# Kernel tuning notes

Hardware: AMD Instinct MI355X
Metric: run time of the kernel (lower is better)

Reference implementation:

```python
import jax, jax.numpy as jnp
import numpy as np

B, T, F, H = 128, 512, 256, 512


def setup_inputs() -> dict:
    key = jax.random.key(0)
    k1, k2, k3, k4 = jax.random.split(key, 4)
    scale_k = 1.0 / np.sqrt(F)
    scale_r = 1.0 / np.sqrt(H)
    return {
        "x": jax.random.normal(k1, (B, T, F), dtype=jnp.float32),
        "kernel": jax.random.normal(k2, (F, 4 * H), dtype=jnp.float32) * scale_k,
        "recurrent_kernel": jax.random.normal(k3, (H, 4 * H), dtype=jnp.float32) * scale_r,
        "bias": jax.random.normal(k4, (4 * H,), dtype=jnp.float32) * 0.01,
    }


def _lstm(x, kernel, recurrent_kernel, bias):
    # x: [B, T, F] -> scan over time. Keras gate order: i, f, g(cell), o.
    h0 = jnp.zeros((x.shape[0], H), dtype=x.dtype)
    c0 = jnp.zeros((x.shape[0], H), dtype=x.dtype)
    # Precompute input projections for all timesteps in one big GEMM: [B,T,4H]
    xz = jnp.einsum('btf,fg->btg', x, kernel) + bias

    def step(carry, xz_t):
        h, c = carry
        z = xz_t + h @ recurrent_kernel  # [B, 4H]
        i, f, g, o = jnp.split(z, 4, axis=-1)
        i = jax.nn.sigmoid(i)
        f = jax.nn.sigmoid(f)
        g = jnp.tanh(g)
        o = jax.nn.sigmoid(o)
        c_new = f * c + i * g
        h_new = o * jnp.tanh(c_new)
        return (h_new, c_new), h_new

    (h_last, c_last), hs = jax.lax.scan(step, (h0, c0), jnp.swapaxes(xz, 0, 1))
    output = jnp.swapaxes(hs, 0, 1)  # [B, T, H]
    return output, h_last, c_last


def reference(x, kernel, recurrent_kernel, bias):
    # Inference-mode forward (dropout inactive), matching Keras LSTM eval behavior.
    output, h, c = _lstm(x, kernel, recurrent_kernel, bias)
    return (output, h, c)
```

## Files before the change

kernel.cpp:

```cpp
#include <hip/hip_runtime.h>
#include <stdint.h>


#define Bb 128
#define Tt 512
#define Ff 256
#define Hh 512
#define G4 2048
#define SENT 0xFFFFFFFFu

typedef __attribute__((ext_vector_type(8))) short short8;
typedef __attribute__((ext_vector_type(4))) float floatx4;
typedef __attribute__((ext_vector_type(4))) unsigned int uint4v;

__device__ __forceinline__ unsigned short f2bf(float f) {
    unsigned u = __float_as_uint(f);
    return (unsigned short)((u + 0x7FFFu + ((u >> 16) & 1u)) >> 16);
}
__device__ __forceinline__ float bf2f(unsigned short h) {
    return __uint_as_float(((unsigned)h) << 16);
}
__device__ __forceinline__ float sigm(float x) { return 1.f / (1.f + __expf(-x)); }
__device__ __forceinline__ float tanh_f(float x) {
    float e = __expf(-2.f * fabsf(x));
    return copysignf((1.f - e) / (1.f + e), x);
}

__global__ __launch_bounds__(256, 2) void lstm_xz(
    const float* __restrict__ x, const float* __restrict__ w,
    const float* __restrict__ bias, _Float16* __restrict__ xzh)
{
    __shared__ unsigned short Ahi[128 * 40];
    __shared__ unsigned short Alo[128 * 40];
    __shared__ unsigned short Wt [128 * 40];

    const int tid = threadIdx.x;
    int idx = blockIdx.x;
    int xcd = idx & 7;
    int chunk = idx >> 3;
    int msup = chunk >> 7;
    int s = chunk & 127;
    int nt = s >> 3;
    int mi0 = s & 7;
    int mt = xcd * 64 + msup * 8 + mi0;
    const int m0 = mt << 7;
    const int n0 = nt << 7;

    const int lane = tid & 63;
    const int wv = tid >> 6;
    const int wm = wv >> 1, wn = wv & 1;
    const int cB = lane & 15, kgrp = lane >> 4;

    floatx4 acc[4][4];
#pragma unroll
    for (int i = 0; i < 4; ++i)
#pragma unroll
        for (int j = 0; j < 4; ++j) acc[i][j] = (floatx4){0.f, 0.f, 0.f, 0.f};

    float bv[4];
#pragma unroll
    for (int ni = 0; ni < 4; ++ni) bv[ni] = bias[n0 + wn * 64 + ni * 16 + cB];

    for (int it = 0; it < 8; ++it) {
        const int k0 = it * 32;
#pragma unroll
        for (int sw = 0; sw < 4; ++sw) {
            int e = sw * 256 + tid;
            int row = e >> 3, kq = e & 7;
            float4 v = *((const float4*)(x + (size_t)(m0 + row) * Ff + k0) + kq);
            unsigned short h0 = f2bf(v.x), h1 = f2bf(v.y), h2 = f2bf(v.z), h3 = f2bf(v.w);
            unsigned short l0 = f2bf(v.x - bf2f(h0)), l1 = f2bf(v.y - bf2f(h1));
            unsigned short l2 = f2bf(v.z - bf2f(h2)), l3 = f2bf(v.w - bf2f(h3));
            uint2 ph, pl;
            ph.x = (unsigned)h0 | ((unsigned)h1 << 16); ph.y = (unsigned)h2 | ((unsigned)h3 << 16);
            pl.x = (unsigned)l0 | ((unsigned)l1 << 16); pl.y = (unsigned)l2 | ((unsigned)l3 << 16);
            *(uint2*)(&Ahi[row * 40 + kq * 4]) = ph;
            *(uint2*)(&Alo[row * 40 + kq * 4]) = pl;
        }
#pragma unroll
        for (int sw = 0; sw < 4; ++sw) {
            int e = sw * 256 + tid;
            int kr = e >> 5, nq = e & 31;
            float4 v = *((const float4*)(w + (size_t)(k0 + kr) * G4 + n0) + nq);
            int nb = nq * 4;
            Wt[(nb + 0) * 40 + kr] = f2bf(v.x);
            Wt[(nb + 1) * 40 + kr] = f2bf(v.y);
            Wt[(nb + 2) * 40 + kr] = f2bf(v.z);
            Wt[(nb + 3) * 40 + kr] = f2bf(v.w);
        }
        __syncthreads();

        short8 bfr[4];
#pragma unroll
        for (int ni = 0; ni < 4; ++ni)
            bfr[ni] = *(const short8*)(&Wt[(wn * 64 + ni * 16 + cB) * 40 + kgrp * 8]);
#pragma unroll
        for (int mi = 0; mi < 4; ++mi) {
            short8 ah = *(const short8*)(&Ahi[(wm * 64 + mi * 16 + cB) * 40 + kgrp * 8]);
            short8 al = *(const short8*)(&Alo[(wm * 64 + mi * 16 + cB) * 40 + kgrp * 8]);
#pragma unroll
            for (int ni = 0; ni < 4; ++ni) {
                acc[mi][ni] = __builtin_amdgcn_mfma_f32_16x16x32_bf16(ah, bfr[ni], acc[mi][ni], 0, 0, 0);
                acc[mi][ni] = __builtin_amdgcn_mfma_f32_16x16x32_bf16(al, bfr[ni], acc[mi][ni], 0, 0, 0);
            }
        }
        __syncthreads();
    }
#pragma unroll
    for (int mi = 0; mi < 4; ++mi)
#pragma unroll
        for (int ni = 0; ni < 4; ++ni) {
            int rowb = m0 + wm * 64 + mi * 16 + kgrp * 4;
            int col = n0 + wn * 64 + ni * 16 + cB;
#pragma unroll
            for (int rr = 0; rr < 4; ++rr)
                xzh[(size_t)(rowb + rr) * G4 + col] = (_Float16)(acc[mi][ni][rr] + bv[ni]);
        }
}

__global__ __launch_bounds__(256, 1) void lstm_rec(
    const _Float16* __restrict__ xzh, const float* __restrict__ rk,
    unsigned* __restrict__ hbuf_u, float* __restrict__ out)
{
    __shared__ unsigned short Rlds[128 * 512];
    __shared__ unsigned short hlds[16 * 512];

    const int tid = threadIdx.x;
    const int idx = blockIdx.x;
    const int rg = idx & 7;
    const int cb = idx >> 3;
    const int b0 = rg * 16;
    const int hc0 = cb * 32;

    const int lane = tid & 63;
    const int wv = tid >> 6;
    const int cB = lane & 15, kgrp = lane >> 4;
    const int hcw = hc0 + wv * 8;
    const int c7 = cB & 7;
    const int col = hcw + c7;
    const bool hi = (cB & 8) != 0;

    for (int e = tid; e < 64 * 512; e += 256) {
        int p = e & 63, k = e >> 6;
        int n0 = 2 * p;
        int loc = n0 & 31, w = n0 >> 5;
        int gate = ((loc >> 4) << 1) | ((loc >> 3) & 1);
        int gcol = gate * Hh + hc0 + w * 8 + (loc & 7);
        float2 v = *(const float2*)(rk + (size_t)k * G4 + gcol);
        Rlds[n0 * 512 + (k ^ ((n0 & 7) << 3))] = f2bf(v.x);
        Rlds[(n0 + 1) * 512 + (k ^ (((n0 + 1) & 7) << 3))] = f2bf(v.y);
    }

    const unsigned* xz_u = (const unsigned*)xzh;
    const unsigned* pr[4];
#pragma unroll
    for (int r = 0; r < 4; ++r)
        pr[r] = xz_u + ((size_t)(b0 + kgrp * 4 + r) * Tt * G4 + (col & ~1)) / 2;

    float xzr[16];
#pragma unroll
    for (int g = 0; g < 4; ++g)
#pragma unroll
        for (int r = 0; r < 4; ++r) {
            unsigned v = pr[r][g * 256];
            xzr[g * 4 + r] = (float)__builtin_bit_cast(_Float16,
                (unsigned short)((col & 1) ? (v >> 16) : (v & 0xffffu)));
        }
#pragma unroll
    for (int r = 0; r < 4; ++r) pr[r] += G4 / 2;

    __syncthreads();

    short8 bf0[16], bf1[16];
    {
        const int nb = wv * 32;
        const int swz = c7 << 3;
#pragma unroll
        for (int kk = 0; kk < 16; ++kk) {
            int kb = (kk * 32 + kgrp * 8) ^ swz;
            bf0[kk] = *(const short8*)&Rlds[(nb + cB) * 512 + kb];
            bf1[kk] = *(const short8*)&Rlds[(nb + 16 + cB) * 512 + kb];
        }
    }

    float creg[4] = {0.f, 0.f, 0.f, 0.f};
    unsigned* hlds_u = (unsigned*)hlds;
    unsigned* const gbase = hbuf_u + (size_t)rg * 4 * 4096;

    for (int t = 0; t < Tt; ++t) {
        const bool last = (t == Tt - 1);

        unsigned pf[16];
        if (!last) {
#pragma unroll
            for (int g = 0; g < 4; ++g)
#pragma unroll
                for (int r = 0; r < 4; ++r)
                    pf[g * 4 + r] = pr[r][g * 256];
        }

        floatx4 acc0 = (floatx4){0.f, 0.f, 0.f, 0.f};
        floatx4 acc1 = (floatx4){0.f, 0.f, 0.f, 0.f};

        if (t > 0) {
            const unsigned* sb = gbase + ((t - 1) & 3) * 4096;
            const unsigned* p0 = sb + (wv + 0) * 256 + 4 * lane;
            const unsigned* p1 = sb + (wv + 4) * 256 + 4 * lane;
            const unsigned* p2 = sb + (wv + 8) * 256 + 4 * lane;
            const unsigned* p3 = sb + (wv + 12) * 256 + 4 * lane;
            uint4v v0, v1, v2, v3;
            for (;;) {
                asm volatile("global_load_dwordx4 %0, %1, off sc0 sc1" : "=v"(v0) : "v"(p0) : "memory");
                asm volatile("global_load_dwordx4 %0, %1, off sc0 sc1" : "=v"(v1) : "v"(p1) : "memory");
                asm volatile("global_load_dwordx4 %0, %1, off sc0 sc1" : "=v"(v2) : "v"(p2) : "memory");
                asm volatile("global_load_dwordx4 %0, %1, off sc0 sc1" : "=v"(v3) : "v"(p3) : "memory");
                asm volatile("s_waitcnt vmcnt(0)" ::: "memory");
                bool bad = (v0[0] == SENT) | (v0[1] == SENT) | (v0[2] == SENT) | (v0[3] == SENT)
                         | (v1[0] == SENT) | (v1[1] == SENT) | (v1[2] == SENT) | (v1[3] == SENT)
                         | (v2[0] == SENT) | (v2[1] == SENT) | (v2[2] == SENT) | (v2[3] == SENT)
                         | (v3[0] == SENT) | (v3[1] == SENT) | (v3[2] == SENT) | (v3[3] == SENT);
                if (!bad) break;
            }
            __builtin_amdgcn_sched_barrier(0);
            *(uint4v*)(hlds_u + (wv + 0) * 256 + 4 * (lane ^ ((wv + 0) & 7))) = v0;
            *(uint4v*)(hlds_u + (wv + 4) * 256 + 4 * (lane ^ ((wv + 4) & 7))) = v1;
            *(uint4v*)(hlds_u + (wv + 8) * 256 + 4 * (lane ^ ((wv + 8) & 7))) = v2;
            *(uint4v*)(hlds_u + (wv + 12) * 256 + 4 * (lane ^ ((wv + 12) & 7))) = v3;
            __syncthreads();

            if (t >= 2) {
                unsigned* rs = gbase + ((t - 2) & 3) * 4096
                             + (tid >> 4) * 256 + (hc0 >> 1) + (tid & 15);
                __hip_atomic_store(rs, SENT, __ATOMIC_RELAXED, __HIP_MEMORY_SCOPE_AGENT);
            }

            const int swz = c7 << 3;
#pragma unroll
            for (int kk = 0; kk < 16; ++kk) {
                int kb = (kk * 32 + kgrp * 8) ^ swz;
                short8 a = *(const short8*)&hlds[cB * 512 + kb];
                acc0 = __builtin_amdgcn_mfma_f32_16x16x32_bf16(a, bf0[kk], acc0, 0, 0, 0);
                acc1 = __builtin_amdgcn_mfma_f32_16x16x32_bf16(a, bf1[kk], acc1, 0, 0, 0);
            }
        }

        float hv[4];
#pragma unroll
        for (int r = 0; r < 4; ++r) {
            float a0 = acc0[r], a1 = acc1[r];
            float a0x = __shfl_xor(a0, 8);
            float a1x = __shfl_xor(a1, 8);
            float zi = (hi ? a0x : a0) + xzr[0 * 4 + r];
            float zf = (hi ? a0 : a0x) + xzr[1 * 4 + r];
            float zg = (hi ? a1x : a1) + xzr[2 * 4 + r];
            float zo = (hi ? a1 : a1x) + xzr[3 * 4 + r];
            creg[r] = sigm(zf) * creg[r] + sigm(zi) * tanh_f(zg);
            hv[r] = sigm(zo) * tanh_f(creg[r]);
        }

        float hn[4];
#pragma unroll
        for (int r = 0; r < 4; ++r) hn[r] = __shfl_xor(hv[r], 1);
        const bool ew = (!hi && !(cB & 1));

        if (!last) {
            unsigned* wbase = gbase + (t & 3) * 4096;
#pragma unroll
            for (int r = 0; r < 4; ++r) {
                if (ew) {
                    unsigned hp = (unsigned)f2bf(hv[r]) | ((unsigned)f2bf(hn[r]) << 16);
                    __hip_atomic_store(wbase + (kgrp * 4 + r) * 256 + (col >> 1), hp,
                                       __ATOMIC_RELAXED, __HIP_MEMORY_SCOPE_AGENT);
                }
            }
        }

#pragma unroll
        for (int r = 0; r < 4; ++r) {
            if (ew) {
                size_t b = (size_t)(b0 + kgrp * 4 + r);
                *(float2*)(out + (b * Tt + (size_t)t) * Hh + col) = make_float2(hv[r], hn[r]);
            }
        }

        if (last) {
            float* hl = out + (size_t)Bb * Tt * Hh;
            float* cl = hl + (size_t)Bb * Hh;
#pragma unroll
            for (int r = 0; r < 4; ++r) {
                float cn = __shfl_xor(creg[r], 1);
                if (ew) {
                    size_t b = (size_t)(b0 + kgrp * 4 + r);
                    *(float2*)(hl + b * Hh + col) = make_float2(hv[r], hn[r]);
                    *(float2*)(cl + b * Hh + col) = make_float2(creg[r], cn);
                }
            }
            break;
        }

#pragma unroll
        for (int i = 0; i < 16; ++i)
            xzr[i] = (float)__builtin_bit_cast(_Float16,
                (unsigned short)((col & 1) ? (pf[i] >> 16) : (pf[i] & 0xffffu)));
#pragma unroll
        for (int r = 0; r < 4; ++r) pr[r] += G4 / 2;

        __syncthreads();
    }
}

extern "C" void kernel_launch(void* const* d_in, const int* in_sizes, int n_in,
                              void* d_out, int out_size, void* d_ws, size_t ws_size,
                              hipStream_t stream) {
    (void)in_sizes; (void)n_in; (void)out_size; (void)ws_size;
    const float* x    = (const float*)d_in[0];
    const float* w    = (const float*)d_in[1];
    const float* rk   = (const float*)d_in[2];
    const float* bias = (const float*)d_in[3];
    float* out = (float*)d_out;

    char* ws = (char*)d_ws;
    const size_t XZ_BYTES   = (size_t)Bb * Tt * G4 * sizeof(_Float16);
    const size_t HBUF_BYTES = (size_t)8 * 4 * 16 * 256 * 4;

    _Float16* xzh = (_Float16*)ws;
    unsigned* hbuf = (unsigned*)(ws + XZ_BYTES);

    hipMemsetAsync(ws + XZ_BYTES, 0xFF, HBUF_BYTES, stream);

    lstm_xz<<<dim3(8192), dim3(256), 0, stream>>>(x, w, bias, xzh);
    lstm_rec<<<dim3(128), dim3(256), 0, stream>>>(xzh, rk, hbuf, out);
}
```

Measured before the change: 2.203 ms.

## Load h operands directly from global into MFMA registers, drop LDS staging and barriers

Each wave now loads its full 16x512 bf16 h fragment straight from the global exchange buffer into registers in MFMA A-operand layout. This replaces the cooperative load, LDS store and __syncthreads. The per-step block barriers are removed, and sentinel polling becomes a wave-wide __any check. The goal is to cut the LDS round trip and the two block-wide synchronizations on the serial recurrent critical path. In exchange each wave issues four times more global loads (redundantly across the 4 waves) and holds 64 more VGPRs. The sentinel reset indexing was changed to match the new ownership.

```diff
diff --git a/kernel.cpp b/kernel.cpp
--- a/kernel.cpp
+++ b/kernel.cpp
@@ -123,7 +123,6 @@
     unsigned* __restrict__ hbuf_u, float* __restrict__ out)
 {
     __shared__ unsigned short Rlds[128 * 512];
-    __shared__ unsigned short hlds[16 * 512];
 
     const int tid = threadIdx.x;
     const int idx = blockIdx.x;
@@ -184,7 +183,6 @@
     }
 
     float creg[4] = {0.f, 0.f, 0.f, 0.f};
-    unsigned* hlds_u = (unsigned*)hlds;
     unsigned* const gbase = hbuf_u + (size_t)rg * 4 * 4096;
 
     for (int t = 0; t < Tt; ++t) {
@@ -203,42 +201,32 @@
         floatx4 acc1 = (floatx4){0.f, 0.f, 0.f, 0.f};
 
         if (t > 0) {
-            const unsigned* sb = gbase + ((t - 1) & 3) * 4096;
-            const unsigned* p0 = sb + (wv + 0) * 256 + 4 * lane;
-            const unsigned* p1 = sb + (wv + 4) * 256 + 4 * lane;
-            const unsigned* p2 = sb + (wv + 8) * 256 + 4 * lane;
-            const unsigned* p3 = sb + (wv + 12) * 256 + 4 * lane;
-            uint4v v0, v1, v2, v3;
+            const unsigned* sp = gbase + ((t - 1) & 3) * 4096 + cB * 256 + kgrp * 4;
+            uint4v A[16];
             for (;;) {
-                asm volatile("global_load_dwordx4 %0, %1, off sc0 sc1" : "=v"(v0) : "v"(p0) : "memory");
-                asm volatile("global_load_dwordx4 %0, %1, off sc0 sc1" : "=v"(v1) : "v"(p1) : "memory");
-                asm volatile("global_load_dwordx4 %0, %1, off sc0 sc1" : "=v"(v2) : "v"(p2) : "memory");
-                asm volatile("global_load_dwordx4 %0, %1, off sc0 sc1" : "=v"(v3) : "v"(p3) : "memory");
+#pragma unroll
+                for (int kk = 0; kk < 16; ++kk)
+                    asm volatile("global_load_dwordx4 %0, %1, off sc0 sc1"
+                                 : "=v"(A[kk]) : "v"(sp + kk * 16) : "memory");
                 asm volatile("s_waitcnt vmcnt(0)" ::: "memory");
-                bool bad = (v0[0] == SENT) | (v0[1] == SENT) | (v0[2] == SENT) | (v0[3] == SENT)
-                         | (v1[0] == SENT) | (v1[1] == SENT) | (v1[2] == SENT) | (v1[3] == SENT)
-                         | (v2[0] == SENT) | (v2[1] == SENT) | (v2[2] == SENT) | (v2[3] == SENT)
-                         | (v3[0] == SENT) | (v3[1] == SENT) | (v3[2] == SENT) | (v3[3] == SENT);
-                if (!bad) break;
-            }
-            __builtin_amdgcn_sched_barrier(0);
-            *(uint4v*)(hlds_u + (wv + 0) * 256 + 4 * (lane ^ ((wv + 0) & 7))) = v0;
-            *(uint4v*)(hlds_u + (wv + 4) * 256 + 4 * (lane ^ ((wv + 4) & 7))) = v1;
-            *(uint4v*)(hlds_u + (wv + 8) * 256 + 4 * (lane ^ ((wv + 8) & 7))) = v2;
-            *(uint4v*)(hlds_u + (wv + 12) * 256 + 4 * (lane ^ ((wv + 12) & 7))) = v3;
-            __syncthreads();
+                __builtin_amdgcn_sched_barrier(0);
+                bool bad = false;
+#pragma unroll
+                for (int kk = 0; kk < 16; ++kk)
+                    bad = bad | (A[kk][0] == SENT) | (A[kk][1] == SENT)
+                              | (A[kk][2] == SENT) | (A[kk][3] == SENT);
+                if (!__any(bad)) break;
+            }
 
             if (t >= 2) {
                 unsigned* rs = gbase + ((t - 2) & 3) * 4096
-                             + (tid >> 4) * 256 + (hc0 >> 1) + (tid & 15);
+                             + (lane >> 2) * 256 + (hc0 >> 1) + wv * 4 + (lane & 3);
                 __hip_atomic_store(rs, SENT, __ATOMIC_RELAXED, __HIP_MEMORY_SCOPE_AGENT);
             }
 
-            const int swz = c7 << 3;
 #pragma unroll
             for (int kk = 0; kk < 16; ++kk) {
-                int kb = (kk * 32 + kgrp * 8) ^ swz;
-                short8 a = *(const short8*)&hlds[cB * 512 + kb];
+                short8 a = __builtin_bit_cast(short8, A[kk]);
                 acc0 = __builtin_amdgcn_mfma_f32_16x16x32_bf16(a, bf0[kk], acc0, 0, 0, 0);
                 acc1 = __builtin_amdgcn_mfma_f32_16x16x32_bf16(a, bf1[kk], acc1, 0, 0, 0);
             }
@@ -304,8 +292,6 @@
                 (unsigned short)((col & 1) ? (pf[i] >> 16) : (pf[i] & 0xffffu)));
 #pragma unroll
         for (int r = 0; r < 4; ++r) pr[r] += G4 / 2;
-
-        __syncthreads();
     }
 }
 
```

Measured after the change: 4.503 ms. 2.04x slower.
